# Kernel tuning notes

Hardware: AMD Instinct MI355X
Metric: run time of the kernel (lower is better)

Reference implementation:

```python
import jax, jax.numpy as jnp
import numpy as np

N_NODES = 50000
N_EDGES = 800000
N_GRAPHS = 512
IN_CH, H, OUT = 58, 64, 128
HEADS1 = 4
NEG_SLOPE = 0.2
BN_EPS = 1e-5


def setup_inputs() -> dict:
    key = jax.random.key(0)
    ks = jax.random.split(key, 16)
    x = jax.random.normal(ks[0], (N_NODES, IN_CH), dtype=jnp.float32)
    edge_index = jax.random.randint(ks[1], (2, N_EDGES), 0, N_NODES, dtype=jnp.int64)
    batch = jnp.sort(jax.random.randint(ks[2], (N_NODES,), 0, N_GRAPHS, dtype=jnp.int64))
    s = 0.1
    return {
        "x": x,
        "edge_index": edge_index,
        "batch": batch,
        "W1": jax.random.normal(ks[3], (IN_CH, HEADS1 * H), dtype=jnp.float32) * s,
        "att_src1": jax.random.normal(ks[4], (HEADS1, H), dtype=jnp.float32) * s,
        "att_dst1": jax.random.normal(ks[5], (HEADS1, H), dtype=jnp.float32) * s,
        "b1": jnp.zeros((HEADS1 * H,), dtype=jnp.float32),
        "W2": jax.random.normal(ks[6], (HEADS1 * H, OUT), dtype=jnp.float32) * s,
        "att_src2": jax.random.normal(ks[7], (1, OUT), dtype=jnp.float32) * s,
        "att_dst2": jax.random.normal(ks[8], (1, OUT), dtype=jnp.float32) * s,
        "b2": jnp.zeros((OUT,), dtype=jnp.float32),
        "gamma": jax.random.normal(ks[9], (OUT,), dtype=jnp.float32) * 0.1 + 1.0,
        "beta": jax.random.normal(ks[10], (OUT,), dtype=jnp.float32) * 0.1,
    }


def gat_conv(x, src, dst, W, att_src, att_dst, b, heads, d_out):
    """PyG GATConv (concat=True, dropout off), self-loops already in src/dst."""
    n = x.shape[0]
    h = (x @ W).reshape(n, heads, d_out)                 # [N,H,D]
    a_s = jnp.einsum("nhd,hd->nh", h, att_src)            # [N,H]
    a_d = jnp.einsum("nhd,hd->nh", h, att_dst)            # [N,H]
    e = jax.nn.leaky_relu(a_s[src] + a_d[dst], NEG_SLOPE)  # [E,H]
    # softmax over edges grouped by destination node
    m = jax.ops.segment_max(e, dst, num_segments=n)
    ex = jnp.exp(e - m[dst])
    z = jax.ops.segment_sum(ex, dst, num_segments=n)
    alpha = ex / (z[dst] + 1e-16)
    msg = h[src] * alpha[:, :, None]                      # [E,H,D]
    out = jax.ops.segment_sum(msg, dst, num_segments=n)   # [N,H,D]
    return out.reshape(n, heads * d_out) + b


def reference(x, edge_index, batch, W1, att_src1, att_dst1, b1,
              W2, att_src2, att_dst2, b2, gamma, beta):
    n = x.shape[0]
    loops = jnp.arange(n, dtype=edge_index.dtype)
    src = jnp.concatenate([edge_index[0], loops])
    dst = jnp.concatenate([edge_index[1], loops])

    h1 = jax.nn.relu(gat_conv(x, src, dst, W1, att_src1, att_dst1, b1, HEADS1, H))
    h2 = jax.nn.relu(gat_conv(h1, src, dst, W2, att_src2, att_dst2, b2, 1, OUT))

    # global mean pool over graphs
    sums = jax.ops.segment_sum(h2, batch, num_segments=N_GRAPHS)      # [G,OUT]
    cnt = jax.ops.segment_sum(jnp.ones((n,), h2.dtype), batch, num_segments=N_GRAPHS)
    pooled = sums / jnp.maximum(cnt, 1.0)[:, None]

    # BatchNorm1d, training mode (batch statistics, biased variance)
    mu = pooled.mean(axis=0)
    var = pooled.var(axis=0)
    return (pooled - mu) / jnp.sqrt(var + BN_EPS) * gamma + beta
```

## Files before the change

kernel.cpp:

```cpp
#include <hip/hip_runtime.h>
#include <hip/hip_bf16.h>
#include <math.h>

#define N_NODES  50000
#define N_EDGES  800000
#define E_TOT    850000
#define N_GRAPHS 512
#define IN_CH    58
#define K1P      64
#define C1       256
#define H1       4
#define C2       128
#define NEG_SLOPE 0.2f
#define SLOT_CAP 64
#define NBUILD   208
#define NATT     3125
#define NBUCK    196
#define BCAP     5120

typedef __attribute__((ext_vector_type(8))) short short8;
typedef __attribute__((ext_vector_type(4))) float f32x4;

__device__ __forceinline__ float lo16(unsigned u) { return __uint_as_float(u << 16); }
__device__ __forceinline__ float hi16(unsigned u) { return __uint_as_float(u & 0xffff0000u); }
__device__ __forceinline__ float leaky(float e) { return e > 0.f ? e : NEG_SLOPE * e; }
__device__ __forceinline__ unsigned short f2bfu(float v) {
    __hip_bfloat16 b = __float2bfloat16(v);
    return *(unsigned short*)&b;
}
__device__ __forceinline__ unsigned pack2(float lo, float hi) {
    return (unsigned)f2bfu(lo) | ((unsigned)f2bfu(hi) << 16);
}

__global__ __launch_bounds__(256) void k_frontA(const float* __restrict__ W1,
                                                const float* __restrict__ W2,
                                                const float* __restrict__ atts1,
                                                const float* __restrict__ attd1,
                                                unsigned short* __restrict__ w1p,
                                                unsigned short* __restrict__ w2p,
                                                float* __restrict__ wproj) {
    int b = blockIdx.x;
    int t = threadIdx.x;
    if (b < 256) {
        if (t < K1P) {
            float v = (t < IN_CH) ? W1[t * C1 + b] : 0.f;
            int h = b >> 6, jj = (b >> 4) & 3, l15 = b & 15;
            int kk = t >> 5, quad = (t >> 3) & 3, e = t & 7;
            int f = (h * 4 + jj) * 2 + kk;
            w1p[(f * 64 + l15 * 4 + quad) * 8 + e] = f2bfu(v);
        }
    } else if (b < 384) {
        int n = b - 256;
        int j = n >> 4, l15 = n & 15;
        int k0 = t >> 5, quad = (t >> 3) & 3, e = t & 7;
        int f = j * 8 + k0;
        w2p[(f * 64 + l15 * 4 + quad) * 8 + e] = f2bfu(W2[t * C2 + n]);
    } else {
        int k = t >> 2, h = t & 3;
        float s = 0.f, dd = 0.f;
        if (k < IN_CH) {
            for (int j = 0; j < 64; ++j) {
                float wv = W1[k * C1 + h * 64 + j];
                s  += wv * atts1[h * 64 + j];
                dd += wv * attd1[h * 64 + j];
            }
        }
        wproj[t] = s;
        wproj[256 + t] = dd;
    }
}

__global__ __launch_bounds__(256) void k_mid(const int* __restrict__ src,
                                             const int* __restrict__ dst,
                                             int* __restrict__ bcnt,
                                             uint2* __restrict__ ebuf,
                                             const float* __restrict__ x,
                                             const float* __restrict__ wproj,
                                             unsigned short* __restrict__ xbf,
                                             float* __restrict__ a_s,
                                             float* __restrict__ a_d) {
    __shared__ int lhist[NBUCK];
    __shared__ int lbase[NBUCK];
    int b = blockIdx.x;
    int t = threadIdx.x;
    if (b < NBUILD) {
        if (t < NBUCK) lhist[t] = 0;
        __syncthreads();
        int j0 = (b * 256 + t) * 16;
        int s[16], d[16], bk[16], lp[16];
        bool v[16];
#pragma unroll
        for (int k = 0; k < 16; ++k) {
            int j = j0 + k;
            v[k] = j < E_TOT;
            if (v[k]) {
                if (j < N_EDGES) { s[k] = src[j]; d[k] = dst[j]; }
                else             { s[k] = d[k] = j - N_EDGES; }
                bk[k] = d[k] >> 8;
            }
        }
#pragma unroll
        for (int k = 0; k < 16; ++k)
            if (v[k]) lp[k] = atomicAdd(&lhist[bk[k]], 1);
        __syncthreads();
        if (t < NBUCK) lbase[t] = atomicAdd(&bcnt[t], lhist[t]);
        __syncthreads();
#pragma unroll
        for (int k = 0; k < 16; ++k)
            if (v[k])
                ebuf[(size_t)bk[k] * BCAP + lbase[bk[k]] + lp[k]] =
                    make_uint2((unsigned)s[k], (unsigned)d[k]);
    } else {
        int wave = t >> 6, lane = t & 63;
        int q = lane >> 4, hl = lane & 15;
        int n = (b - NBUILD) * 16 + wave * 4 + q;
        float xa[4] = {0.f, 0.f, 0.f, 0.f};
        const float* xr = x + (size_t)n * IN_CH + hl * 4;
        if (hl < 14) {
            float4 xv = *(const float4*)xr;
            xa[0] = xv.x; xa[1] = xv.y; xa[2] = xv.z; xa[3] = xv.w;
        } else if (hl == 14) {
            xa[0] = xr[0]; xa[1] = xr[1];
        }
        ((uint2*)xbf)[n * 16 + hl] = make_uint2(pack2(xa[0], xa[1]), pack2(xa[2], xa[3]));
        float ps[4] = {0.f, 0.f, 0.f, 0.f}, pd[4] = {0.f, 0.f, 0.f, 0.f};
#pragma unroll
        for (int cc = 0; cc < 4; ++cc) {
            int c = hl * 4 + cc;
            float4 wsv = *(const float4*)(wproj + c * 4);
            float4 wdv = *(const float4*)(wproj + 256 + c * 4);
            ps[0] += xa[cc] * wsv.x; ps[1] += xa[cc] * wsv.y;
            ps[2] += xa[cc] * wsv.z; ps[3] += xa[cc] * wsv.w;
            pd[0] += xa[cc] * wdv.x; pd[1] += xa[cc] * wdv.y;
            pd[2] += xa[cc] * wdv.z; pd[3] += xa[cc] * wdv.w;
        }
#pragma unroll
        for (int o = 8; o > 0; o >>= 1) {
#pragma unroll
            for (int r = 0; r < 4; ++r) {
                ps[r] += __shfl_down(ps[r], o, 16);
                pd[r] += __shfl_down(pd[r], o, 16);
            }
        }
        if (hl == 0) {
            *(float4*)(a_s + n * 4) = make_float4(ps[0], ps[1], ps[2], ps[3]);
            *(float4*)(a_d + n * 4) = make_float4(pd[0], pd[1], pd[2], pd[3]);
        }
    }
}

__global__ __launch_bounds__(256) void k_scat(const int* __restrict__ bcnt,
                                              const uint2* __restrict__ ebuf,
                                              int* __restrict__ deg,
                                              int* __restrict__ slots) {
    __shared__ int ldeg[256];
    int blk = blockIdx.x, t = threadIdx.x;
    ldeg[t] = 0;
    __syncthreads();
    int cnt = bcnt[blk];
    const uint2* eb = ebuf + (size_t)blk * BCAP;
    int base = 0;
    for (; base + 1024 <= cnt; base += 1024) {
        uint2 e[4];
#pragma unroll
        for (int k = 0; k < 4; ++k) e[k] = eb[base + k * 256 + t];
#pragma unroll
        for (int k = 0; k < 4; ++k) {
            int pos = atomicAdd(&ldeg[e[k].y & 255], 1);
            slots[((int)e[k].y << 6) + pos] = (int)e[k].x;
        }
    }
    for (int i = base + t; i < cnt; i += 256) {
        uint2 e = eb[i];
        int pos = atomicAdd(&ldeg[e.y & 255], 1);
        slots[((int)e.y << 6) + pos] = (int)e.x;
    }
    __syncthreads();
    int g = (blk << 8) + t;
    if (g < N_NODES) deg[g] = ldeg[t];
}

__global__ __launch_bounds__(256) void k_l1_agg(const int* __restrict__ degv,
                                                const int* __restrict__ slots,
                                                const float* __restrict__ a_s,
                                                const float* __restrict__ a_d,
                                                const uint2* __restrict__ xbf,
                                                unsigned short* __restrict__ xagg) {
    int t = threadIdx.x;
    int wave = t >> 6, lane = t & 63;
    int q = lane >> 4, hl = lane & 15;
    int d = blockIdx.x * 16 + wave * 4 + q;
    int beg = d << 6;
    int dg = degv[d];
    float4 ad = *(const float4*)(a_d + d * 4);
    float z0 = 0.f, z1 = 0.f, z2 = 0.f, z3 = 0.f;
    float a0[4] = {0.f, 0.f, 0.f, 0.f};
    float a1[4] = {0.f, 0.f, 0.f, 0.f};
    float a2[4] = {0.f, 0.f, 0.f, 0.f};
    float a3[4] = {0.f, 0.f, 0.f, 0.f};
    int s0 = slots[beg];
    int nit = (dg + 7) >> 3;
    int s[8];
#pragma unroll
    for (int k = 0; k < 8; ++k) s[k] = (k < dg) ? slots[beg + k] : s0;
    for (int it = 0; it < nit; ++it) {
        int ibase = it * 8;
        int sn[8];
#pragma unroll
        for (int k = 0; k < 8; ++k) {
            int idx = ibase + 8 + k;
            int raw = slots[beg + (idx & 63)];
            sn[k] = (idx < dg) ? raw : s0;
        }
        uint2 u[8]; float4 as[8];
#pragma unroll
        for (int k = 0; k < 8; ++k) u[k] = xbf[s[k] * 16 + hl];
#pragma unroll
        for (int k = 0; k < 8; ++k) as[k] = *(const float4*)(a_s + s[k] * 4);
#pragma unroll
        for (int k = 0; k < 8; ++k) {
            bool val = (ibase + k) < dg;
            float e0h = val ? __expf(leaky(as[k].x + ad.x)) : 0.f;
            float e1h = val ? __expf(leaky(as[k].y + ad.y)) : 0.f;
            float e2h = val ? __expf(leaky(as[k].z + ad.z)) : 0.f;
            float e3h = val ? __expf(leaky(as[k].w + ad.w)) : 0.f;
            z0 += e0h; z1 += e1h; z2 += e2h; z3 += e3h;
            float c0 = lo16(u[k].x), c1 = hi16(u[k].x);
            float c2 = lo16(u[k].y), c3 = hi16(u[k].y);
            a0[0] += e0h * c0; a0[1] += e0h * c1; a0[2] += e0h * c2; a0[3] += e0h * c3;
            a1[0] += e1h * c0; a1[1] += e1h * c1; a1[2] += e1h * c2; a1[3] += e1h * c3;
            a2[0] += e2h * c0; a2[1] += e2h * c1; a2[2] += e2h * c2; a2[3] += e2h * c3;
            a3[0] += e3h * c0; a3[1] += e3h * c1; a3[2] += e3h * c2; a3[3] += e3h * c3;
        }
#pragma unroll
        for (int k = 0; k < 8; ++k) s[k] = sn[k];
    }
    float i0 = 1.f / z0, i1 = 1.f / z1, i2 = 1.f / z2, i3 = 1.f / z3;
    int T = d >> 4, r = d & 15;
    int kk = hl >> 3, qd = (hl >> 1) & 3, half = hl & 1;
    uint2* xo = (uint2*)xagg;
    int base = (((T * 8 + kk) * 64) + r * 4 + qd) * 2 + half;
    xo[base +   0] = make_uint2(pack2(a0[0] * i0, a0[1] * i0), pack2(a0[2] * i0, a0[3] * i0));
    xo[base + 256] = make_uint2(pack2(a1[0] * i1, a1[1] * i1), pack2(a1[2] * i1, a1[3] * i1));
    xo[base + 512] = make_uint2(pack2(a2[0] * i2, a2[1] * i2), pack2(a2[2] * i2, a2[3] * i2));
    xo[base + 768] = make_uint2(pack2(a3[0] * i3, a3[1] * i3), pack2(a3[2] * i3, a3[3] * i3));
}

__global__ __launch_bounds__(256) void k_gemm12(const unsigned short* __restrict__ xagg,
                                                const unsigned short* __restrict__ w1p,
                                                const float* __restrict__ b1v,
                                                const unsigned short* __restrict__ w2p,
                                                const float* __restrict__ atts,
                                                const float* __restrict__ attd,
                                                unsigned short* __restrict__ h2bf,
                                                float* __restrict__ a_s,
                                                float* __restrict__ a_d) {
    __shared__ unsigned short hlds[4][16][264];
    int t = threadIdx.x;
    int wave = t >> 6, lane = t & 63;
    int T = blockIdx.x * 4 + wave;
    int m0 = T * 16;
    int l15 = lane & 15, quad = lane >> 4;
    int fl = l15 * 4 + quad;
    bool active = m0 < N_NODES;

    if (active) {
        const short8* xf  = (const short8*)xagg + (size_t)T * 512 + fl;
        const short8* w1f = (const short8*)w1p + fl;
        short8 av[H1][2];
#pragma unroll
        for (int h = 0; h < H1; ++h) {
            av[h][0] = xf[(h * 2 + 0) * 64];
            av[h][1] = xf[(h * 2 + 1) * 64];
        }
#pragma unroll
        for (int h = 0; h < H1; ++h) {
            short8 wb0[4], wb1[4];
#pragma unroll
            for (int jj = 0; jj < 4; ++jj) {
                wb0[jj] = w1f[(((h * 4 + jj) * 2) + 0) * 64];
                wb1[jj] = w1f[(((h * 4 + jj) * 2) + 1) * 64];
            }
            f32x4 acc[4];
#pragma unroll
            for (int jj = 0; jj < 4; ++jj) {
                acc[jj] = (f32x4){0.f, 0.f, 0.f, 0.f};
                acc[jj] = __builtin_amdgcn_mfma_f32_16x16x32_bf16(av[h][0], wb0[jj], acc[jj], 0, 0, 0);
                acc[jj] = __builtin_amdgcn_mfma_f32_16x16x32_bf16(av[h][1], wb1[jj], acc[jj], 0, 0, 0);
            }
#pragma unroll
            for (int jj = 0; jj < 4; ++jj) {
                int c = h * 64 + jj * 16 + l15;
                float bb = b1v[c];
#pragma unroll
                for (int r = 0; r < 4; ++r)
                    hlds[wave][quad * 4 + r][c] = f2bfu(fmaxf(acc[jj][r] + bb, 0.f));
            }
        }
    }
    __syncthreads();
    if (!active) return;

    short8 a2[8];
    const unsigned short* a2row = &hlds[wave][l15][0] + quad * 8;
#pragma unroll
    for (int k0 = 0; k0 < 8; ++k0) a2[k0] = *(const short8*)(a2row + k0 * 32);

    const short8* w2f = (const short8*)w2p + fl;
    unsigned short* scr = &hlds[wave][0][0];
    float ps[4] = {0.f, 0.f, 0.f, 0.f}, pd[4] = {0.f, 0.f, 0.f, 0.f};
#pragma unroll
    for (int j = 0; j < 8; ++j) {
        short8 wb[8];
#pragma unroll
        for (int k0 = 0; k0 < 8; ++k0)
            wb[k0] = w2f[(j * 8 + k0) * 64];
        f32x4 acc = (f32x4){0.f, 0.f, 0.f, 0.f};
#pragma unroll
        for (int k0 = 0; k0 < 8; ++k0)
            acc = __builtin_amdgcn_mfma_f32_16x16x32_bf16(a2[k0], wb[k0], acc, 0, 0, 0);
        float as_ = atts[j * 16 + l15], ad_ = attd[j * 16 + l15];
#pragma unroll
        for (int r = 0; r < 4; ++r) {
            float v = acc[r];
            scr[(quad * 4 + r) * 136 + j * 16 + l15] = f2bfu(v);
            ps[r] += v * as_;
            pd[r] += v * ad_;
        }
    }
#pragma unroll
    for (int r = 0; r < 4; ++r) {
#pragma unroll
        for (int o = 8; o > 0; o >>= 1) {
            ps[r] += __shfl_down(ps[r], o, 16);
            pd[r] += __shfl_down(pd[r], o, 16);
        }
        if (l15 == 0) {
            int n = m0 + quad * 4 + r;
            a_s[n] = ps[r];
            a_d[n] = pd[r];
        }
    }
    int row = lane >> 2, seg = lane & 3;
#pragma unroll
    for (int c = 0; c < 4; ++c) {
        short8 v = *(const short8*)(scr + row * 136 + (c * 4 + seg) * 8);
        *(short8*)(h2bf + (size_t)(m0 + row) * C2 + (c * 4 + seg) * 8) = v;
    }
}

__global__ __launch_bounds__(256) void k_l2_aggpool(const int* __restrict__ degv,
                                                    const int* __restrict__ slots,
                                                    const float* __restrict__ a_s,
                                                    const float* __restrict__ a_d,
                                                    const unsigned short* __restrict__ h2bf,
                                                    const float* __restrict__ b2,
                                                    const int* __restrict__ batch,
                                                    float* __restrict__ pooled) {
    __shared__ float sacc[8][C2];
    __shared__ int sg[8];
    __shared__ int sdeg[8];
    __shared__ int perm[8];
    int t = threadIdx.x;
    int wave = t >> 6, lane = t & 63;
    int half = lane >> 5, hl = lane & 31;
    if (t < 8) {
        sdeg[t] = degv[blockIdx.x * 8 + t];
        sg[t] = batch[blockIdx.x * 8 + t];
    }
    __syncthreads();
    if (t < 8) {
        int dgi = sdeg[t], r = 0;
#pragma unroll
        for (int j = 0; j < 8; ++j) {
            int dj = sdeg[j];
            r += (dj < dgi) || (dj == dgi && j < t);
        }
        perm[r] = t;
    }
    __syncthreads();
    int nodeIdx = wave * 2 + half;
    int loc = perm[nodeIdx];
    int d = blockIdx.x * 8 + loc;
    int beg = d << 6;
    int dg = sdeg[loc];
    float ad = a_d[d];
    const uint2* rows = (const uint2*)h2bf;
    float a0 = 0.f, a1 = 0.f, a2 = 0.f, a3 = 0.f, z = 0.f;
    int s0 = slots[beg];
    int nit = (dg + 7) >> 3;
    int s[8];
#pragma unroll
    for (int k = 0; k < 8; ++k) s[k] = (k < dg) ? slots[beg + k] : s0;
    for (int it = 0; it < nit; ++it) {
        int ibase = it * 8;
        int sn[8];
#pragma unroll
        for (int k = 0; k < 8; ++k) {
            int idx = ibase + 8 + k;
            int raw = slots[beg + (idx & 63)];
            sn[k] = (idx < dg) ? raw : s0;
        }
        uint2 u[8]; float ex[8];
#pragma unroll
        for (int k = 0; k < 8; ++k) u[k] = rows[s[k] * 32 + hl];
#pragma unroll
        for (int k = 0; k < 8; ++k) {
            bool val = (ibase + k) < dg;
            ex[k] = val ? __expf(leaky(a_s[s[k]] + ad)) : 0.f;
        }
#pragma unroll
        for (int k = 0; k < 8; ++k) {
            z  += ex[k];
            a0 += ex[k] * lo16(u[k].x); a1 += ex[k] * hi16(u[k].x);
            a2 += ex[k] * lo16(u[k].y); a3 += ex[k] * hi16(u[k].y);
        }
#pragma unroll
        for (int k = 0; k < 8; ++k) s[k] = sn[k];
    }
    float inv = 1.f / z;
    int c = hl * 4;
    float4 bv = *(const float4*)(b2 + c);
    float v0 = fmaxf(a0 * inv + bv.x, 0.f);
    float v1 = fmaxf(a1 * inv + bv.y, 0.f);
    float v2 = fmaxf(a2 * inv + bv.z, 0.f);
    float v3 = fmaxf(a3 * inv + bv.w, 0.f);
    *(float4*)&sacc[loc][c] = make_float4(v0, v1, v2, v3);
    __syncthreads();
    if (t < C2) {
        float run = sacc[0][t];
        int gprev = sg[0];
#pragma unroll
        for (int j = 1; j < 8; ++j) {
            int gj = sg[j];
            float v = sacc[j][t];
            if (gj == gprev) {
                run += v;
            } else {
                atomicAdd(&pooled[gprev * C2 + t], run);
                run = v;
                gprev = gj;
            }
        }
        atomicAdd(&pooled[gprev * C2 + t], run);
    }
}

__global__ __launch_bounds__(512) void k_bn(const float* __restrict__ pooled,
                                            const int* __restrict__ batch,
                                            const float* __restrict__ gamma,
                                            const float* __restrict__ beta,
                                            float* __restrict__ out) {
    int c = blockIdx.x;
    int g = threadIdx.x;
    int lo = 0, hi = N_NODES;
    while (lo < hi) { int m = (lo + hi) >> 1; if (batch[m] < g) lo = m + 1; else hi = m; }
    int lo2 = lo, hi2 = N_NODES;
    while (lo2 < hi2) { int m = (lo2 + hi2) >> 1; if (batch[m] < g + 1) lo2 = m + 1; else hi2 = m; }
    float cntg = (float)(hi2 - lo);

    __shared__ float red[512];
    __shared__ float s_mu, s_var;
    float v = pooled[g * C2 + c] / fmaxf(cntg, 1.0f);
    red[g] = v;
    __syncthreads();
    for (int s = 256; s > 0; s >>= 1) {
        if (g < s) red[g] += red[g + s];
        __syncthreads();
    }
    if (g == 0) s_mu = red[0] * (1.0f / N_GRAPHS);
    __syncthreads();
    float dv = v - s_mu;
    red[g] = dv * dv;
    __syncthreads();
    for (int s = 256; s > 0; s >>= 1) {
        if (g < s) red[g] += red[g + s];
        __syncthreads();
    }
    if (g == 0) s_var = red[0] * (1.0f / N_GRAPHS);
    __syncthreads();
    out[g * C2 + c] = dv * rsqrtf(s_var + 1e-5f) * gamma[c] + beta[c];
}

extern "C" void kernel_launch(void* const* d_in, const int* in_sizes, int n_in,
                              void* d_out, int out_size, void* d_ws, size_t ws_size,
                              hipStream_t stream) {
    const float* x     = (const float*)d_in[0];
    const int*   eidx  = (const int*)d_in[1];
    const int*   batch = (const int*)d_in[2];
    const float* W1    = (const float*)d_in[3];
    const float* atts1 = (const float*)d_in[4];
    const float* attd1 = (const float*)d_in[5];
    const float* b1    = (const float*)d_in[6];
    const float* W2    = (const float*)d_in[7];
    const float* atts2 = (const float*)d_in[8];
    const float* attd2 = (const float*)d_in[9];
    const float* b2    = (const float*)d_in[10];
    const float* gamma = (const float*)d_in[11];
    const float* beta  = (const float*)d_in[12];
    float* out = (float*)d_out;
    float* ws  = (float*)d_ws;

    const int* src = eidx;
    const int* dst = eidx + N_EDGES;

    const size_t o_xbf    = 0;
    const size_t o_xagg   = 1600000;
    const size_t o_h2bf   = 8000000;
    const size_t o_w1p    = 11200000;
    const size_t o_w2p    = 11208192;
    const size_t o_wproj  = 11224576;
    const size_t o_as1    = 11225088;
    const size_t o_ad1    = 11425088;
    const size_t o_as2    = 11625088;
    const size_t o_ad2    = 11675088;
    const size_t o_slots  = 11725088;
    const size_t o_deg    = 14925088;
    const size_t o_pool   = 14975088;
    const size_t o_bcnt   = 15040624;
    const size_t total    = 15040880;

    int* p_slots = (int*)(ws + o_slots);
    int* p_deg   = (int*)(ws + o_deg);
    int* p_bcnt  = (int*)(ws + o_bcnt);
    uint2* p_ebuf = (uint2*)(ws + o_xagg);
    unsigned short* p_xbf  = (unsigned short*)(ws + o_xbf);
    unsigned short* p_xagg = (unsigned short*)(ws + o_xagg);
    unsigned short* p_h2bf = (unsigned short*)(ws + o_h2bf);
    unsigned short* p_w1p  = (unsigned short*)(ws + o_w1p);
    unsigned short* p_w2p  = (unsigned short*)(ws + o_w2p);

    hipMemsetAsync(ws + o_deg, 0, (total - o_deg) * sizeof(float), stream);

    k_frontA<<<385, 256, 0, stream>>>(W1, W2, atts1, attd1,
                                      p_w1p, p_w2p, ws + o_wproj);
    k_mid<<<NBUILD + NATT, 256, 0, stream>>>(src, dst, p_bcnt, p_ebuf,
                                             x, ws + o_wproj, p_xbf,
                                             ws + o_as1, ws + o_ad1);
    k_scat<<<NBUCK, 256, 0, stream>>>(p_bcnt, p_ebuf, p_deg, p_slots);

    const int nagg1 = N_NODES / 16;
    const int nagg2 = N_NODES / 8;
    const int nmfma = (N_NODES + 63) / 64;

    k_l1_agg<<<nagg1, 256, 0, stream>>>(p_deg, p_slots, ws + o_as1, ws + o_ad1,
                                        (const uint2*)p_xbf, p_xagg);
    k_gemm12<<<nmfma, 256, 0, stream>>>(p_xagg, p_w1p, b1, p_w2p, atts2, attd2,
                                        p_h2bf, ws + o_as2, ws + o_ad2);

    k_l2_aggpool<<<nagg2, 256, 0, stream>>>(p_deg, p_slots, ws + o_as2, ws + o_ad2,
                                            p_h2bf, b2, batch, ws + o_pool);

    k_bn<<<C2, 512, 0, stream>>>(ws + o_pool, batch, gamma, beta, out);
}
```

Before: 250.4 us.

## Compute attention weights lane-parallel and broadcast via shuffles in aggregation kernels

In both GAT aggregation kernels, each lane of a 16- or 32-lane group now loads one neighbor slot and computes its exp attention weight. Softmax denominators come from a shuffle reduction, and the weights are normalized before accumulation. Neighbor indices and weights are then broadcast with shuffles while the group gathers feature rows in batches of 16. This removes redundant per-lane slot loads, a_s loads and exp computations across lanes. It assumes degree ≤ 64 (the slot cap) and adds many shuffles per edge.

After: 221.3 us. 11.6% less time.

```diff
diff --git a/kernel.cpp b/kernel.cpp
--- a/kernel.cpp
+++ b/kernel.cpp
@@ -193,57 +193,74 @@
     int beg = d << 6;
     int dg = degv[d];
     float4 ad = *(const float4*)(a_d + d * 4);
-    float z0 = 0.f, z1 = 0.f, z2 = 0.f, z3 = 0.f;
+    int s0 = slots[beg];
+    int sR[4];
+    float w[4][4];
+#pragma unroll
+    for (int g = 0; g < 4; ++g) {
+        int idx = g * 16 + hl;
+        bool val = idx < dg;
+        int raw = val ? slots[beg + idx] : s0;
+        sR[g] = raw;
+        if (val) {
+            float4 as = *(const float4*)(a_s + raw * 4);
+            w[g][0] = __expf(leaky(as.x + ad.x));
+            w[g][1] = __expf(leaky(as.y + ad.y));
+            w[g][2] = __expf(leaky(as.z + ad.z));
+            w[g][3] = __expf(leaky(as.w + ad.w));
+        } else {
+            w[g][0] = 0.f; w[g][1] = 0.f; w[g][2] = 0.f; w[g][3] = 0.f;
+        }
+    }
+    float z[4];
+#pragma unroll
+    for (int h = 0; h < 4; ++h) z[h] = w[0][h] + w[1][h] + w[2][h] + w[3][h];
+#pragma unroll
+    for (int o = 8; o > 0; o >>= 1)
+#pragma unroll
+        for (int h = 0; h < 4; ++h) z[h] += __shfl_xor(z[h], o, 16);
+#pragma unroll
+    for (int h = 0; h < 4; ++h) {
+        float iz = 1.f / z[h];
+#pragma unroll
+        for (int g = 0; g < 4; ++g) w[g][h] *= iz;
+    }
     float a0[4] = {0.f, 0.f, 0.f, 0.f};
     float a1[4] = {0.f, 0.f, 0.f, 0.f};
     float a2[4] = {0.f, 0.f, 0.f, 0.f};
     float a3[4] = {0.f, 0.f, 0.f, 0.f};
-    int s0 = slots[beg];
-    int nit = (dg + 7) >> 3;
-    int s[8];
-#pragma unroll
-    for (int k = 0; k < 8; ++k) s[k] = (k < dg) ? slots[beg + k] : s0;
-    for (int it = 0; it < nit; ++it) {
-        int ibase = it * 8;
-        int sn[8];
-#pragma unroll
-        for (int k = 0; k < 8; ++k) {
-            int idx = ibase + 8 + k;
-            int raw = slots[beg + (idx & 63)];
-            sn[k] = (idx < dg) ? raw : s0;
-        }
-        uint2 u[8]; float4 as[8];
-#pragma unroll
-        for (int k = 0; k < 8; ++k) u[k] = xbf[s[k] * 16 + hl];
-#pragma unroll
-        for (int k = 0; k < 8; ++k) as[k] = *(const float4*)(a_s + s[k] * 4);
-#pragma unroll
-        for (int k = 0; k < 8; ++k) {
-            bool val = (ibase + k) < dg;
-            float e0h = val ? __expf(leaky(as[k].x + ad.x)) : 0.f;
-            float e1h = val ? __expf(leaky(as[k].y + ad.y)) : 0.f;
-            float e2h = val ? __expf(leaky(as[k].z + ad.z)) : 0.f;
-            float e3h = val ? __expf(leaky(as[k].w + ad.w)) : 0.f;
-            z0 += e0h; z1 += e1h; z2 += e2h; z3 += e3h;
-            float c0 = lo16(u[k].x), c1 = hi16(u[k].x);
-            float c2 = lo16(u[k].y), c3 = hi16(u[k].y);
-            a0[0] += e0h * c0; a0[1] += e0h * c1; a0[2] += e0h * c2; a0[3] += e0h * c3;
-            a1[0] += e1h * c0; a1[1] += e1h * c1; a1[2] += e1h * c2; a1[3] += e1h * c3;
-            a2[0] += e2h * c0; a2[1] += e2h * c1; a2[2] += e2h * c2; a2[3] += e2h * c3;
-            a3[0] += e3h * c0; a3[1] += e3h * c1; a3[2] += e3h * c2; a3[3] += e3h * c3;
-        }
-#pragma unroll
-        for (int k = 0; k < 8; ++k) s[k] = sn[k];
-    }
-    float i0 = 1.f / z0, i1 = 1.f / z1, i2 = 1.f / z2, i3 = 1.f / z3;
+#pragma unroll
+    for (int g = 0; g < 4; ++g) {
+        if (g * 16 < dg) {
+            int sk[16];
+#pragma unroll
+            for (int kk = 0; kk < 16; ++kk) sk[kk] = __shfl(sR[g], kk, 16);
+            uint2 u[16];
+#pragma unroll
+            for (int kk = 0; kk < 16; ++kk) u[kk] = xbf[sk[kk] * 16 + hl];
+#pragma unroll
+            for (int kk = 0; kk < 16; ++kk) {
+                float w0 = __shfl(w[g][0], kk, 16);
+                float w1 = __shfl(w[g][1], kk, 16);
+                float w2 = __shfl(w[g][2], kk, 16);
+                float w3 = __shfl(w[g][3], kk, 16);
+                float c0 = lo16(u[kk].x), c1 = hi16(u[kk].x);
+                float c2 = lo16(u[kk].y), c3 = hi16(u[kk].y);
+                a0[0] += w0 * c0; a0[1] += w0 * c1; a0[2] += w0 * c2; a0[3] += w0 * c3;
+                a1[0] += w1 * c0; a1[1] += w1 * c1; a1[2] += w1 * c2; a1[3] += w1 * c3;
+                a2[0] += w2 * c0; a2[1] += w2 * c1; a2[2] += w2 * c2; a2[3] += w2 * c3;
+                a3[0] += w3 * c0; a3[1] += w3 * c1; a3[2] += w3 * c2; a3[3] += w3 * c3;
+            }
+        }
+    }
     int T = d >> 4, r = d & 15;
     int kk = hl >> 3, qd = (hl >> 1) & 3, half = hl & 1;
     uint2* xo = (uint2*)xagg;
     int base = (((T * 8 + kk) * 64) + r * 4 + qd) * 2 + half;
-    xo[base +   0] = make_uint2(pack2(a0[0] * i0, a0[1] * i0), pack2(a0[2] * i0, a0[3] * i0));
-    xo[base + 256] = make_uint2(pack2(a1[0] * i1, a1[1] * i1), pack2(a1[2] * i1, a1[3] * i1));
-    xo[base + 512] = make_uint2(pack2(a2[0] * i2, a2[1] * i2), pack2(a2[2] * i2, a2[3] * i2));
-    xo[base + 768] = make_uint2(pack2(a3[0] * i3, a3[1] * i3), pack2(a3[2] * i3, a3[3] * i3));
+    xo[base +   0] = make_uint2(pack2(a0[0], a0[1]), pack2(a0[2], a0[3]));
+    xo[base + 256] = make_uint2(pack2(a1[0], a1[1]), pack2(a1[2], a1[3]));
+    xo[base + 512] = make_uint2(pack2(a2[0], a2[1]), pack2(a2[2], a2[3]));
+    xo[base + 768] = make_uint2(pack2(a3[0], a3[1]), pack2(a3[2], a3[3]));
 }
 
 __global__ __launch_bounds__(256) void k_gemm12(const unsigned short* __restrict__ xagg,
@@ -386,45 +403,46 @@
     int dg = sdeg[loc];
     float ad = a_d[d];
     const uint2* rows = (const uint2*)h2bf;
-    float a0 = 0.f, a1 = 0.f, a2 = 0.f, a3 = 0.f, z = 0.f;
     int s0 = slots[beg];
-    int nit = (dg + 7) >> 3;
-    int s[8];
-#pragma unroll
-    for (int k = 0; k < 8; ++k) s[k] = (k < dg) ? slots[beg + k] : s0;
-    for (int it = 0; it < nit; ++it) {
-        int ibase = it * 8;
-        int sn[8];
-#pragma unroll
-        for (int k = 0; k < 8; ++k) {
-            int idx = ibase + 8 + k;
-            int raw = slots[beg + (idx & 63)];
-            sn[k] = (idx < dg) ? raw : s0;
-        }
-        uint2 u[8]; float ex[8];
-#pragma unroll
-        for (int k = 0; k < 8; ++k) u[k] = rows[s[k] * 32 + hl];
-#pragma unroll
-        for (int k = 0; k < 8; ++k) {
-            bool val = (ibase + k) < dg;
-            ex[k] = val ? __expf(leaky(a_s[s[k]] + ad)) : 0.f;
-        }
-#pragma unroll
-        for (int k = 0; k < 8; ++k) {
-            z  += ex[k];
-            a0 += ex[k] * lo16(u[k].x); a1 += ex[k] * hi16(u[k].x);
-            a2 += ex[k] * lo16(u[k].y); a3 += ex[k] * hi16(u[k].y);
-        }
-#pragma unroll
-        for (int k = 0; k < 8; ++k) s[k] = sn[k];
-    }
-    float inv = 1.f / z;
+    int sR[2]; float w[2];
+#pragma unroll
+    for (int g = 0; g < 2; ++g) {
+        int idx = g * 32 + hl;
+        bool val = idx < dg;
+        int raw = val ? slots[beg + idx] : s0;
+        sR[g] = raw;
+        w[g] = val ? __expf(leaky(a_s[raw] + ad)) : 0.f;
+    }
+    float z = w[0] + w[1];
+#pragma unroll
+    for (int o = 16; o > 0; o >>= 1) z += __shfl_xor(z, o, 32);
+    float iz = 1.f / z;
+    w[0] *= iz; w[1] *= iz;
+    float a0 = 0.f, a1 = 0.f, a2 = 0.f, a3 = 0.f;
+#pragma unroll
+    for (int m = 0; m < 4; ++m) {
+        if (m * 16 < dg) {
+            const int g = m >> 1, off = (m & 1) * 16;
+            int sk[16];
+#pragma unroll
+            for (int kk = 0; kk < 16; ++kk) sk[kk] = __shfl(sR[g], off + kk, 32);
+            uint2 u[16];
+#pragma unroll
+            for (int kk = 0; kk < 16; ++kk) u[kk] = rows[sk[kk] * 32 + hl];
+#pragma unroll
+            for (int kk = 0; kk < 16; ++kk) {
+                float wk = __shfl(w[g], off + kk, 32);
+                a0 += wk * lo16(u[kk].x); a1 += wk * hi16(u[kk].x);
+                a2 += wk * lo16(u[kk].y); a3 += wk * hi16(u[kk].y);
+            }
+        }
+    }
     int c = hl * 4;
     float4 bv = *(const float4*)(b2 + c);
-    float v0 = fmaxf(a0 * inv + bv.x, 0.f);
-    float v1 = fmaxf(a1 * inv + bv.y, 0.f);
-    float v2 = fmaxf(a2 * inv + bv.z, 0.f);
-    float v3 = fmaxf(a3 * inv + bv.w, 0.f);
+    float v0 = fmaxf(a0 + bv.x, 0.f);
+    float v1 = fmaxf(a1 + bv.y, 0.f);
+    float v2 = fmaxf(a2 + bv.z, 0.f);
+    float v3 = fmaxf(a3 + bv.w, 0.f);
     *(float4*)&sacc[loc][c] = make_float4(v0, v1, v2, v3);
     __syncthreads();
     if (t < C2) {
```
